# Performance work log

Hardware: AMD Instinct MI355X
Metric: run time of the kernel (lower is better)

The kernel has to match this reference:

```python
import jax, jax.numpy as jnp
import numpy as np

# CTBG circuit dims: units=[512,512,512], action_sz=6
UNIT1, UNIT2, UNIT3, ACTION = 512, 512, 512, 6
D_GPE_IN = UNIT1 * 3          # 1536  (striatum D1/D2/D3 blocks)
D_GPE_OUT = UNIT2 * 3         # 1536
D_GPI_IN = (UNIT1 + UNIT2) * 3  # 3072 (striatum + GPe/STN blocks)
D_GPI_OUT = UNIT2 * 3         # 1536
B = 16384


def setup_inputs() -> dict:
    key = jax.random.key(0)
    ks = jax.random.split(key, 12)
    x = jax.random.normal(ks[0], (B, D_GPE_IN), jnp.float32)
    # per-unit diagonal connectivity masks (unit_diags): [units, input_dim]
    gpe_mask = jax.random.bernoulli(ks[1], 0.5, (D_GPE_OUT, D_GPE_IN)).astype(jnp.float32)
    gpi_mask = jax.random.bernoulli(ks[2], 0.5, (D_GPI_OUT, D_GPI_IN)).astype(jnp.float32)
    # non-negative weights, uniform [0, 0.01) as in the TF initializer
    gpe_w = jax.random.uniform(ks[3], (D_GPE_IN, D_GPE_OUT), jnp.float32, 0.0, 0.01)
    gpe_b = jnp.zeros((D_GPE_OUT,), jnp.float32)
    gpi_w = jax.random.uniform(ks[4], (D_GPI_IN, D_GPI_OUT), jnp.float32, 0.0, 0.01)
    gpi_b = jnp.zeros((D_GPI_OUT,), jnp.float32)
    # Motor_cortex dense stack
    w1 = jax.random.normal(ks[5], (D_GPI_OUT, UNIT3), jnp.float32) / np.sqrt(D_GPI_OUT)
    b1 = jnp.zeros((UNIT3,), jnp.float32)
    w2 = jax.random.normal(ks[6], (UNIT3, UNIT3), jnp.float32) / np.sqrt(UNIT3)
    b2 = jnp.zeros((UNIT3,), jnp.float32)
    w3 = jax.random.normal(ks[7], (UNIT3, ACTION), jnp.float32) / np.sqrt(UNIT3)
    b3 = jnp.zeros((ACTION,), jnp.float32)
    return {"x": x, "gpe_mask": gpe_mask, "gpe_w": gpe_w, "gpe_b": gpe_b,
            "gpi_mask": gpi_mask, "gpi_w": gpi_w, "gpi_b": gpi_b,
            "w1": w1, "b1": b1, "w2": w2, "b2": b2, "w3": w3, "b3": b3}


def _masked_layer(x, mask, w, b):
    # TF original: p = transpose(matmul(diag(mask_u), x^T)) -> [B,U,I];
    #              f = diag_part(matmul(p, w)) + b
    # algebraically: f[b,u] = sum_i mask[u,i] * x[b,i] * w[i,u] + b[u]
    # which is a plain matmul against the element-wise masked weight.
    return x @ (w * mask.T) + b


def reference(x, gpe_mask, gpe_w, gpe_b, gpi_mask, gpi_w, gpi_b,
              w1, b1, w2, b2, w3, b3):
    gpe_out = _masked_layer(x, gpe_mask, gpe_w, gpe_b)          # [B, 1536]
    gpi_in = jnp.concatenate([x, gpe_out], axis=-1)              # [B, 3072]
    gpi_out = _masked_layer(gpi_in, gpi_mask, gpi_w, gpi_b)      # [B, 1536]
    h = jax.nn.relu(gpi_out @ w1 + b1)
    h = jax.nn.relu(h @ w2 + b2)
    return jax.nn.relu(h @ w3 + b3)                              # [B, 6]
```

## Files before the change

### kernel.cpp

```cpp
#include <hip/hip_runtime.h>
#include <stdint.h>


typedef __attribute__((ext_vector_type(8))) short short8;
typedef __attribute__((ext_vector_type(4))) float floatx4;

typedef const __attribute__((address_space(1))) void* gas1_cvp;
typedef __attribute__((address_space(3))) void* gas3_vp;

__device__ __forceinline__ void load_lds16(const void* g, void* s) {
    __builtin_amdgcn_global_load_lds((gas1_cvp)g, (gas3_vp)s, 16, 0, 0);
}

__device__ __forceinline__ unsigned short f2bf(float f) {
    unsigned int u = __float_as_uint(f);
    u = u + 0x7fffu + ((u >> 16) & 1u);
    return (unsigned short)(u >> 16);
}
__device__ __forceinline__ float bf2f(unsigned short h) {
    return __uint_as_float(((unsigned int)h) << 16);
}
__device__ __forceinline__ short8 cvt8(float4 a, float4 b) {
    short8 r;
    r[0] = (short)f2bf(a.x); r[1] = (short)f2bf(a.y);
    r[2] = (short)f2bf(a.z); r[3] = (short)f2bf(a.w);
    r[4] = (short)f2bf(b.x); r[5] = (short)f2bf(b.y);
    r[6] = (short)f2bf(b.z); r[7] = (short)f2bf(b.w);
    return r;
}

__device__ __forceinline__ void dev_prep_t(
        float (*tile)[65],
        const float* __restrict__ w, const float* __restrict__ mask,
        unsigned short* __restrict__ out,
        int ldw, int ldm, int ldo, int bx, int by) {
    int n0 = bx * 64;
    int k0 = by * 64;
    int t = threadIdx.x;
    int c4 = (t & 15) * 4;
    int r  = t >> 4;

    #pragma unroll
    for (int p = 0; p < 4; ++p) {
        int kk = r + p * 16;
        float4 v = *(const float4*)(w + (size_t)(k0 + kk) * ldw + n0 + c4);
        tile[c4 + 0][kk] = v.x;
        tile[c4 + 1][kk] = v.y;
        tile[c4 + 2][kk] = v.z;
        tile[c4 + 3][kk] = v.w;
    }
    __syncthreads();
    #pragma unroll
    for (int p = 0; p < 4; ++p) {
        int nn = r + p * 16;
        float mx = 1.f, my = 1.f, mz = 1.f, mw = 1.f;
        if (mask) {
            float4 m = *(const float4*)(mask + (size_t)(n0 + nn) * ldm + k0 + c4);
            mx = m.x; my = m.y; mz = m.z; mw = m.w;
        }
        ushort4 o;
        o.x = f2bf(tile[nn][c4 + 0] * mx);
        o.y = f2bf(tile[nn][c4 + 1] * my);
        o.z = f2bf(tile[nn][c4 + 2] * mz);
        o.w = f2bf(tile[nn][c4 + 3] * mw);
        *(ushort4*)(out + (size_t)(n0 + nn) * ldo + k0 + c4) = o;
    }
}

__device__ __forceinline__ void dev_prep_nt(
        float (*tile)[65],
        const float* __restrict__ w, const float* __restrict__ mask,
        unsigned short* __restrict__ out,
        int ldw, int ldm, int ldo, int bx, int by) {
    int j0 = bx * 64;
    int i0 = by * 64;
    int t = threadIdx.x;
    int c4 = (t & 15) * 4;
    int r  = t >> 4;

    #pragma unroll
    for (int p = 0; p < 4; ++p) {
        int jj = r + p * 16;
        float4 m = *(const float4*)(mask + (size_t)(j0 + jj) * ldm + i0 + c4);
        tile[c4 + 0][jj] = m.x;
        tile[c4 + 1][jj] = m.y;
        tile[c4 + 2][jj] = m.z;
        tile[c4 + 3][jj] = m.w;
    }
    __syncthreads();
    #pragma unroll
    for (int p = 0; p < 4; ++p) {
        int ii = r + p * 16;
        float4 v = *(const float4*)(w + (size_t)(i0 + ii) * ldw + j0 + c4);
        ushort4 o;
        o.x = f2bf(v.x * tile[ii][c4 + 0]);
        o.y = f2bf(v.y * tile[ii][c4 + 1]);
        o.z = f2bf(v.z * tile[ii][c4 + 2]);
        o.w = f2bf(v.w * tile[ii][c4 + 3]);
        *(ushort4*)(out + (size_t)(i0 + ii) * ldo + j0 + c4) = o;
    }
}

__global__ __launch_bounds__(256) void prep_all_kernel(
        const float* __restrict__ gpe_w, const float* __restrict__ gpe_mask,
        const float* __restrict__ gpi_w, const float* __restrict__ gpi_mask,
        const float* __restrict__ w1, const float* __restrict__ w2,
        unsigned short* __restrict__ wi_topnt, unsigned short* __restrict__ wibot_ui,
        unsigned short* __restrict__ we_nt, unsigned short* __restrict__ w1t,
        unsigned short* __restrict__ w2t) {
    __shared__ float tile[64][65];
    int b = blockIdx.x;
    if (b < 576) {
        dev_prep_nt(tile, gpi_w, gpi_mask, wi_topnt, 1536, 3072, 1536,
                    b % 24, b / 24);
    } else if (b < 1152) {
        int lb = b - 576;
        dev_prep_nt(tile, gpi_w + (size_t)1536 * 1536, gpi_mask + 1536, wibot_ui,
                    1536, 3072, 1536, lb % 24, lb / 24);
    } else if (b < 1728) {
        int lb = b - 1152;
        dev_prep_nt(tile, gpe_w, gpe_mask, we_nt, 1536, 1536, 1536,
                    lb % 24, lb / 24);
    } else if (b < 1920) {
        int lb = b - 1728;
        dev_prep_t(tile, w1, nullptr, w1t, 512, 0, 1536, lb % 8, lb / 8);
    } else {
        int lb = b - 1920;
        dev_prep_t(tile, w2, nullptr, w2t, 512, 0, 512, lb % 8, lb / 8);
    }
}

__device__ __forceinline__ void dev_combine_pipe(
        unsigned short* As, unsigned short* Bs,
        const unsigned short* __restrict__ A0,
        const unsigned short* __restrict__ B0,
        const unsigned short* __restrict__ A1,
        const unsigned short* __restrict__ B1,
        unsigned short* __restrict__ C,
        int nt0, int ntTot, int bx, int by) {
    const int m0 = by * 64;
    const int n0 = bx * 128;
    const int t    = threadIdx.x;
    const int lane = t & 63;
    const int w    = t >> 6;
    const int wm   = w >> 1;
    const int wn   = w & 1;
    const int lm   = lane & 15;
    const int lq   = lane >> 4;

    const int srow = lane >> 2;
    const int scol = (lane & 3) * 8;

    size_t ag_off[2];
    int rbA[2];
    #pragma unroll
    for (int i = 0; i < 2; ++i) {
        ag_off[i] = (size_t)(m0 + w * 16 + srow) * 1536 + i * 32 + scol;
        rbA[i]    = i * 2048 + w * 512;
    }
    size_t bg_off[4];
    int rbB[4];
    #pragma unroll
    for (int i = 0; i < 4; ++i) {
        int rows = w * 32 + (i >> 1) * 16;
        bg_off[i] = (size_t)(n0 + rows + srow) * 1536 + (i & 1) * 32 + scol;
        rbB[i]    = (i & 1) * 4096 + rows * 32;
    }

    int aro[2][2], bro[2][4];
    #pragma unroll
    for (int ks = 0; ks < 2; ++ks) {
        #pragma unroll
        for (int mi = 0; mi < 2; ++mi)
            aro[ks][mi] = ks * 2048 + (wm * 32 + mi * 16 + lm) * 32 + lq * 8;
        #pragma unroll
        for (int ni = 0; ni < 4; ++ni)
            bro[ks][ni] = ks * 4096 + (wn * 64 + ni * 16 + lm) * 32 + lq * 8;
    }

    floatx4 acc[2][4] = {};

    auto stage = [&](int s, int nb) {
        const unsigned short* Ab;
        const unsigned short* Bb;
        int kk;
        if (s < nt0) { Ab = A0; Bb = B0; kk = s << 6; }
        else         { Ab = A1; Bb = B1; kk = (s - nt0) << 6; }
        #pragma unroll
        for (int i = 0; i < 2; ++i)
            load_lds16(Ab + ag_off[i] + kk, As + nb * 4096 + rbA[i]);
        #pragma unroll
        for (int i = 0; i < 4; ++i)
            load_lds16(Bb + bg_off[i] + kk, Bs + nb * 8192 + rbB[i]);
    };

    stage(0, 0);
    __syncthreads();

    int buf = 0;
    for (int tt = 0; tt < ntTot; ++tt) {
        if (tt + 1 < ntTot) stage(tt + 1, buf ^ 1);
        const int cA = buf * 4096, cB = buf * 8192;
        #pragma unroll
        for (int ks = 0; ks < 2; ++ks) {
            short8 af[2], bf8[4];
            #pragma unroll
            for (int mi = 0; mi < 2; ++mi)
                af[mi] = *(const short8*)(As + cA + aro[ks][mi]);
            #pragma unroll
            for (int ni = 0; ni < 4; ++ni)
                bf8[ni] = *(const short8*)(Bs + cB + bro[ks][ni]);
            #pragma unroll
            for (int mi = 0; mi < 2; ++mi)
                #pragma unroll
                for (int ni = 0; ni < 4; ++ni)
                    acc[mi][ni] = __builtin_amdgcn_mfma_f32_16x16x32_bf16(
                        af[mi], bf8[ni], acc[mi][ni], 0, 0, 0);
        }
        if (tt + 1 < ntTot) __syncthreads();
        buf ^= 1;
    }

    #pragma unroll
    for (int mi = 0; mi < 2; ++mi) {
        int rbase = m0 + wm * 32 + mi * 16 + lq * 4;
        #pragma unroll
        for (int ni = 0; ni < 4; ++ni) {
            int cc = n0 + wn * 64 + ni * 16 + lm;
            #pragma unroll
            for (int r = 0; r < 4; ++r)
                C[(size_t)(rbase + r) * 1536 + cc] = f2bf(acc[mi][ni][r]);
        }
    }
}

__global__ __launch_bounds__(256) void combineA_kernel(
        const unsigned short* __restrict__ w1t,
        const unsigned short* __restrict__ wibot_ui,
        unsigned short* __restrict__ t1) {
    __shared__ unsigned short As[2 * 4096];
    __shared__ unsigned short Bs[2 * 8192];
    int b = blockIdx.x;
    dev_combine_pipe(As, Bs, w1t, wibot_ui, w1t, wibot_ui, t1,
                     24, 24, b % 12, b / 12);
}

__device__ __forceinline__ void dev_bvec2(
        const float* __restrict__ gpi_b, const float* __restrict__ gpe_b,
        const unsigned short* __restrict__ w1t,
        const unsigned short* __restrict__ t1,
        const float* __restrict__ b1, float* __restrict__ b1c, int blk) {
    int n = blk * 4 + (threadIdx.x >> 6);
    int lane = threadIdx.x & 63;
    const unsigned short* r1 = w1t + (size_t)n * 1536;
    const unsigned short* r2 = t1  + (size_t)n * 1536;
    float s = 0.f;
    for (int i = lane; i < 1536; i += 64)
        s += gpi_b[i] * bf2f(r1[i]) + gpe_b[i] * bf2f(r2[i]);
    #pragma unroll
    for (int off = 32; off; off >>= 1) s += __shfl_down(s, off, 64);
    if (lane == 0) b1c[n] = b1[n] + s;
}

__global__ __launch_bounds__(256) void combineB_kernel(
        const unsigned short* __restrict__ w1t,
        const unsigned short* __restrict__ wi_topnt,
        const unsigned short* __restrict__ t1,
        const unsigned short* __restrict__ we_nt,
        unsigned short* __restrict__ w1ct,
        const float* __restrict__ gpi_b, const float* __restrict__ gpe_b,
        const float* __restrict__ b1, float* __restrict__ b1c) {
    __shared__ unsigned short As[2 * 4096];
    __shared__ unsigned short Bs[2 * 8192];
    int b = blockIdx.x;
    if (b < 96) {
        dev_combine_pipe(As, Bs, w1t, wi_topnt, t1, we_nt, w1ct,
                         24, 48, b % 12, b / 12);
    } else {
        dev_bvec2(gpi_b, gpe_b, w1t, t1, b1, b1c, b - 96);
    }
}

__global__ __launch_bounds__(256) void gemm_a32_kernel(
        const float* __restrict__ A,
        const unsigned short* __restrict__ Bt,
        const float* __restrict__ bias,
        unsigned short* __restrict__ C,
        int K, int lda, int ldc) {
    __shared__ unsigned short As[2 * 8192];
    __shared__ unsigned short Bs[2 * 8192];

    const int bid = blockIdx.x;
    const int loc = bid >> 3;
    const int m0 = ((bid & 7) * 16 + (loc >> 2)) * 128;
    const int n0 = (loc & 3) * 128;

    const int t    = threadIdx.x;
    const int lane = t & 63;
    const int w    = t >> 6;
    const int wm   = w >> 1;
    const int wn   = w & 1;
    const int lm   = lane & 15;
    const int lq   = lane >> 4;

    const int srow = lane >> 2;
    const int scol = (lane & 3) * 8;

    const float* ag[4];
    const unsigned short* bg[4];
    int rb[4];
    int awr[4];
    #pragma unroll
    for (int i = 0; i < 4; ++i) {
        int rows = w * 32 + (i >> 1) * 16;
        ag[i]  = A  + (size_t)(m0 + rows + srow) * lda + (i & 1) * 32 + scol;
        bg[i]  = Bt + (size_t)(n0 + rows + srow) * K   + (i & 1) * 32 + scol;
        rb[i]  = (i & 1) * 4096 + rows * 32;
        awr[i] = (i & 1) * 4096 + (rows + srow) * 32 + scol;
    }

    int aro[2][4], bro[2][4];
    #pragma unroll
    for (int ks = 0; ks < 2; ++ks)
        #pragma unroll
        for (int i = 0; i < 4; ++i) {
            aro[ks][i] = ks * 4096 + (wm * 64 + i * 16 + lm) * 32 + lq * 8;
            bro[ks][i] = ks * 4096 + (wn * 64 + i * 16 + lm) * 32 + lq * 8;
        }

    floatx4 acc[4][4] = {};
    float4 ra[4][2];

    #pragma unroll
    for (int i = 0; i < 4; ++i) load_lds16(bg[i], Bs + rb[i]);
    #pragma unroll
    for (int i = 0; i < 4; ++i) {
        ra[i][0] = *(const float4*)(ag[i]);
        ra[i][1] = *(const float4*)(ag[i] + 4);
    }
    #pragma unroll
    for (int i = 0; i < 4; ++i)
        *(short8*)(As + awr[i]) = cvt8(ra[i][0], ra[i][1]);
    __syncthreads();

    const int nt = K >> 6;
    int buf = 0;
    for (int tt = 0; tt < nt; ++tt) {
        const int kn = (tt + 1) << 6;
        const int more = kn < K;
        if (more) {
            const int nb = (buf ^ 1) * 8192;
            #pragma unroll
            for (int i = 0; i < 4; ++i)
                load_lds16(bg[i] + kn, Bs + nb + rb[i]);
            #pragma unroll
            for (int i = 0; i < 4; ++i) {
                ra[i][0] = *(const float4*)(ag[i] + kn);
                ra[i][1] = *(const float4*)(ag[i] + kn + 4);
            }
        }
        const int cb = buf * 8192;
        #pragma unroll
        for (int ks = 0; ks < 2; ++ks) {
            short8 af[4], bf8[4];
            #pragma unroll
            for (int i = 0; i < 4; ++i) {
                af[i]  = *(const short8*)(As + cb + aro[ks][i]);
                bf8[i] = *(const short8*)(Bs + cb + bro[ks][i]);
            }
            #pragma unroll
            for (int mi = 0; mi < 4; ++mi)
                #pragma unroll
                for (int ni = 0; ni < 4; ++ni)
                    acc[mi][ni] = __builtin_amdgcn_mfma_f32_16x16x32_bf16(
                        af[mi], bf8[ni], acc[mi][ni], 0, 0, 0);
        }
        if (more) {
            const int nb = (buf ^ 1) * 8192;
            #pragma unroll
            for (int i = 0; i < 4; ++i)
                *(short8*)(As + nb + awr[i]) = cvt8(ra[i][0], ra[i][1]);
            __syncthreads();
        }
        buf ^= 1;
    }

    float bv[4];
    #pragma unroll
    for (int ni = 0; ni < 4; ++ni) bv[ni] = bias[n0 + wn * 64 + ni * 16 + lm];

    #pragma unroll
    for (int mi = 0; mi < 4; ++mi) {
        int rbase = m0 + wm * 64 + mi * 16 + lq * 4;
        #pragma unroll
        for (int ni = 0; ni < 4; ++ni) {
            int cc = n0 + wn * 64 + ni * 16 + lm;
            #pragma unroll
            for (int r = 0; r < 4; ++r) {
                float v = fmaxf(acc[mi][ni][r] + bv[ni], 0.f);
                C[(size_t)(rbase + r) * ldc + cc] = f2bf(v);
            }
        }
    }
}

__global__ __launch_bounds__(256) void gemm_bt_kernel(
        const unsigned short* __restrict__ A,
        const unsigned short* __restrict__ Bt,
        const float* __restrict__ bias,
        unsigned short* __restrict__ C,
        int K, int lda, int ldc) {
    __shared__ unsigned short As[2 * 8192];
    __shared__ unsigned short Bs[2 * 8192];

    const int bid = blockIdx.x;
    const int loc = bid >> 3;
    const int m0 = ((bid & 7) * 16 + (loc >> 2)) * 128;
    const int n0 = (loc & 3) * 128;

    const int t    = threadIdx.x;
    const int lane = t & 63;
    const int w    = t >> 6;
    const int wm   = w >> 1;
    const int wn   = w & 1;
    const int lm   = lane & 15;
    const int lq   = lane >> 4;

    const int srow = lane >> 2;
    const int scol = (lane & 3) * 8;

    const unsigned short* ag[4];
    const unsigned short* bg[4];
    int rb[4];
    #pragma unroll
    for (int i = 0; i < 4; ++i) {
        int rows = w * 32 + (i >> 1) * 16;
        ag[i] = A  + (size_t)(m0 + rows + srow) * lda + (i & 1) * 32 + scol;
        bg[i] = Bt + (size_t)(n0 + rows + srow) * K   + (i & 1) * 32 + scol;
        rb[i] = (i & 1) * 4096 + rows * 32;
    }

    int aro[2][4], bro[2][4];
    #pragma unroll
    for (int ks = 0; ks < 2; ++ks)
        #pragma unroll
        for (int i = 0; i < 4; ++i) {
            aro[ks][i] = ks * 4096 + (wm * 64 + i * 16 + lm) * 32 + lq * 8;
            bro[ks][i] = ks * 4096 + (wn * 64 + i * 16 + lm) * 32 + lq * 8;
        }

    floatx4 acc[4][4] = {};

    #pragma unroll
    for (int i = 0; i < 4; ++i) {
        load_lds16(ag[i], As + rb[i]);
        load_lds16(bg[i], Bs + rb[i]);
    }
    __syncthreads();

    const int nt = K >> 6;
    int buf = 0;
    for (int tt = 0; tt < nt; ++tt) {
        const int kn = (tt + 1) << 6;
        const int more = kn < K;
        if (more) {
            const int nb = (buf ^ 1) * 8192;
            #pragma unroll
            for (int i = 0; i < 4; ++i) {
                load_lds16(ag[i] + kn, As + nb + rb[i]);
                load_lds16(bg[i] + kn, Bs + nb + rb[i]);
            }
        }
        const int cb = buf * 8192;
        #pragma unroll
        for (int ks = 0; ks < 2; ++ks) {
            short8 af[4], bf8[4];
            #pragma unroll
            for (int i = 0; i < 4; ++i) {
                af[i]  = *(const short8*)(As + cb + aro[ks][i]);
                bf8[i] = *(const short8*)(Bs + cb + bro[ks][i]);
            }
            #pragma unroll
            for (int mi = 0; mi < 4; ++mi)
                #pragma unroll
                for (int ni = 0; ni < 4; ++ni)
                    acc[mi][ni] = __builtin_amdgcn_mfma_f32_16x16x32_bf16(
                        af[mi], bf8[ni], acc[mi][ni], 0, 0, 0);
        }
        if (more) __syncthreads();
        buf ^= 1;
    }

    float bv[4];
    #pragma unroll
    for (int ni = 0; ni < 4; ++ni) bv[ni] = bias[n0 + wn * 64 + ni * 16 + lm];

    #pragma unroll
    for (int mi = 0; mi < 4; ++mi) {
        int rbase = m0 + wm * 64 + mi * 16 + lq * 4;
        #pragma unroll
        for (int ni = 0; ni < 4; ++ni) {
            int cc = n0 + wn * 64 + ni * 16 + lm;
            #pragma unroll
            for (int r = 0; r < 4; ++r) {
                float v = fmaxf(acc[mi][ni][r] + bv[ni], 0.f);
                C[(size_t)(rbase + r) * ldc + cc] = f2bf(v);
            }
        }
    }
}

__global__ void head_kernel(const unsigned short* __restrict__ h,
                            const float* __restrict__ w3,
                            const float* __restrict__ b3,
                            float* __restrict__ out) {
    int row = blockIdx.x * 4 + (threadIdx.x >> 6);
    int lane = threadIdx.x & 63;
    const unsigned short* hp = h + (size_t)row * 512 + lane * 8;
    ushort4 ha = *(const ushort4*)(hp);
    ushort4 hb = *(const ushort4*)(hp + 4);
    float hv[8] = {bf2f(ha.x), bf2f(ha.y), bf2f(ha.z), bf2f(ha.w),
                   bf2f(hb.x), bf2f(hb.y), bf2f(hb.z), bf2f(hb.w)};
    const float* wp = w3 + lane * 48;
    float s[6] = {0.f, 0.f, 0.f, 0.f, 0.f, 0.f};
    #pragma unroll
    for (int j = 0; j < 8; ++j)
        #pragma unroll
        for (int a = 0; a < 6; ++a)
            s[a] += hv[j] * wp[j * 6 + a];
    #pragma unroll
    for (int a = 0; a < 6; ++a)
        #pragma unroll
        for (int off = 32; off; off >>= 1)
            s[a] += __shfl_down(s[a], off, 64);
    if (lane == 0) {
        #pragma unroll
        for (int a = 0; a < 6; ++a)
            out[(size_t)row * 6 + a] = fmaxf(s[a] + b3[a], 0.f);
    }
}

extern "C" void kernel_launch(void* const* d_in, const int* in_sizes, int n_in,
                              void* d_out, int out_size, void* d_ws, size_t ws_size,
                              hipStream_t stream) {
    const float* x        = (const float*)d_in[0];
    const float* gpe_mask = (const float*)d_in[1];
    const float* gpe_w    = (const float*)d_in[2];
    const float* gpe_b    = (const float*)d_in[3];
    const float* gpi_mask = (const float*)d_in[4];
    const float* gpi_w    = (const float*)d_in[5];
    const float* gpi_b    = (const float*)d_in[6];
    const float* w1       = (const float*)d_in[7];
    const float* b1       = (const float*)d_in[8];
    const float* w2       = (const float*)d_in[9];
    const float* b2       = (const float*)d_in[10];
    const float* w3       = (const float*)d_in[11];
    const float* b3       = (const float*)d_in[12];
    float* out = (float*)d_out;

    char* ws = (char*)d_ws;
    unsigned short* h1        = (unsigned short*)(ws);
    unsigned short* h2        = (unsigned short*)(ws + 16777216);
    unsigned short* wi_topnt  = (unsigned short*)(ws + 33554432);
    unsigned short* wibot_ui  = (unsigned short*)(ws + 38273024);
    unsigned short* we_nt     = (unsigned short*)(ws + 42991616);
    unsigned short* t1        = (unsigned short*)(ws + 47710208);
    unsigned short* w1t       = (unsigned short*)(ws + 49283072);
    unsigned short* w2t       = (unsigned short*)(ws + 50855936);
    unsigned short* w1ct      = (unsigned short*)(ws + 51380224);
    float*          b1c       = (float*)(ws + 52953088);

    prep_all_kernel<<<dim3(1984), dim3(256), 0, stream>>>(
        gpe_w, gpe_mask, gpi_w, gpi_mask, w1, w2,
        wi_topnt, wibot_ui, we_nt, w1t, w2t);

    combineA_kernel<<<dim3(96), dim3(256), 0, stream>>>(w1t, wibot_ui, t1);

    combineB_kernel<<<dim3(224), dim3(256), 0, stream>>>(
        w1t, wi_topnt, t1, we_nt, w1ct, gpi_b, gpe_b, b1, b1c);

    gemm_a32_kernel<<<dim3(512), dim3(256), 0, stream>>>(
        x, w1ct, b1c, h1, 1536, 1536, 512);
    gemm_bt_kernel<<<dim3(512), dim3(256), 0, stream>>>(
        h1, w2t, b2, h2, 512, 512, 512);
    head_kernel<<<dim3(16384 / 4), dim3(256), 0, stream>>>(h2, w3, b3, out);
}
```

Baseline: 346.3 us.

## Split-K the weight-combine GEMMs with fp32 atomic accumulation and finalize pass

The weight-folding GEMMs (combineA/combineB) launched only 96 blocks over a long K loop, leaving most CUs idle. They are now split along K into 512-wide chunks (288 and 576 blocks) that accumulate into fp32 buffers with atomic adds. The buffers are zeroed by extra blocks in the prep kernel, and a new finalize kernel converts the result to bf16 and computes the folded bias. The t1 intermediate stays in fp32 and is converted to bf16 when loaded into LDS. This costs an extra launch, atomic traffic and fp32 scratch memory, and makes the summation order nondeterministic.

```diff
diff --git a/kernel.cpp b/kernel.cpp
--- a/kernel.cpp
+++ b/kernel.cpp
@@ -107,7 +107,7 @@
         const float* __restrict__ w1, const float* __restrict__ w2,
         unsigned short* __restrict__ wi_topnt, unsigned short* __restrict__ wibot_ui,
         unsigned short* __restrict__ we_nt, unsigned short* __restrict__ w1t,
-        unsigned short* __restrict__ w2t) {
+        unsigned short* __restrict__ w2t, float* __restrict__ zero_base) {
     __shared__ float tile[64][65];
     int b = blockIdx.x;
     if (b < 576) {
@@ -124,20 +124,24 @@
     } else if (b < 1920) {
         int lb = b - 1728;
         dev_prep_t(tile, w1, nullptr, w1t, 512, 0, 1536, lb % 8, lb / 8);
-    } else {
+    } else if (b < 1984) {
         int lb = b - 1920;
         dev_prep_t(tile, w2, nullptr, w2t, 512, 0, 512, lb % 8, lb / 8);
-    }
-}
-
-__device__ __forceinline__ void dev_combine_pipe(
+    } else {
+        float4 z = {0.f, 0.f, 0.f, 0.f};
+        float* p = zero_base + (size_t)(b - 1984) * 4096 + threadIdx.x * 16;
+        #pragma unroll
+        for (int i = 0; i < 4; ++i) *(float4*)(p + i * 4) = z;
+    }
+}
+
+template <bool F32A>
+__device__ __forceinline__ void dev_combine_splitk(
         unsigned short* As, unsigned short* Bs,
-        const unsigned short* __restrict__ A0,
-        const unsigned short* __restrict__ B0,
-        const unsigned short* __restrict__ A1,
-        const unsigned short* __restrict__ B1,
-        unsigned short* __restrict__ C,
-        int nt0, int ntTot, int bx, int by) {
+        const void* __restrict__ Aop,
+        const unsigned short* __restrict__ B,
+        float* __restrict__ C,
+        int kbase, int ntl, int bx, int by) {
     const int m0 = by * 64;
     const int n0 = bx * 128;
     const int t    = threadIdx.x;
@@ -151,20 +155,21 @@
     const int srow = lane >> 2;
     const int scol = (lane & 3) * 8;
 
-    size_t ag_off[2];
-    int rbA[2];
+    size_t aidx[2];
+    int rbA[2], awr[2];
     #pragma unroll
     for (int i = 0; i < 2; ++i) {
-        ag_off[i] = (size_t)(m0 + w * 16 + srow) * 1536 + i * 32 + scol;
-        rbA[i]    = i * 2048 + w * 512;
-    }
-    size_t bg_off[4];
+        aidx[i] = (size_t)(m0 + w * 16 + srow) * 1536 + i * 32 + scol + kbase;
+        rbA[i]  = i * 2048 + w * 512;
+        awr[i]  = i * 2048 + (w * 16 + srow) * 32 + scol;
+    }
+    size_t bidx[4];
     int rbB[4];
     #pragma unroll
     for (int i = 0; i < 4; ++i) {
         int rows = w * 32 + (i >> 1) * 16;
-        bg_off[i] = (size_t)(n0 + rows + srow) * 1536 + (i & 1) * 32 + scol;
-        rbB[i]    = (i & 1) * 4096 + rows * 32;
+        bidx[i] = (size_t)(n0 + rows + srow) * 1536 + (i & 1) * 32 + scol + kbase;
+        rbB[i]  = (i & 1) * 4096 + rows * 32;
     }
 
     int aro[2][2], bro[2][4];
@@ -178,28 +183,51 @@
             bro[ks][ni] = ks * 4096 + (wn * 64 + ni * 16 + lm) * 32 + lq * 8;
     }
 
+    const float* Af = (const float*)Aop;
+    const unsigned short* Ab = (const unsigned short*)Aop;
+
     floatx4 acc[2][4] = {};
-
-    auto stage = [&](int s, int nb) {
-        const unsigned short* Ab;
-        const unsigned short* Bb;
-        int kk;
-        if (s < nt0) { Ab = A0; Bb = B0; kk = s << 6; }
-        else         { Ab = A1; Bb = B1; kk = (s - nt0) << 6; }
+    float4 ra[2][2];
+
+    #pragma unroll
+    for (int i = 0; i < 4; ++i) load_lds16(B + bidx[i], Bs + rbB[i]);
+    if (F32A) {
+        #pragma unroll
+        for (int i = 0; i < 2; ++i) {
+            ra[i][0] = *(const float4*)(Af + aidx[i]);
+            ra[i][1] = *(const float4*)(Af + aidx[i] + 4);
+        }
         #pragma unroll
         for (int i = 0; i < 2; ++i)
-            load_lds16(Ab + ag_off[i] + kk, As + nb * 4096 + rbA[i]);
-        #pragma unroll
-        for (int i = 0; i < 4; ++i)
-            load_lds16(Bb + bg_off[i] + kk, Bs + nb * 8192 + rbB[i]);
-    };
-
-    stage(0, 0);
+            *(short8*)(As + awr[i]) = cvt8(ra[i][0], ra[i][1]);
+    } else {
+        #pragma unroll
+        for (int i = 0; i < 2; ++i) load_lds16(Ab + aidx[i], As + rbA[i]);
+    }
     __syncthreads();
 
     int buf = 0;
-    for (int tt = 0; tt < ntTot; ++tt) {
-        if (tt + 1 < ntTot) stage(tt + 1, buf ^ 1);
+    for (int tt = 0; tt < ntl; ++tt) {
+        const int kn = (tt + 1) << 6;
+        const int more = tt + 1 < ntl;
+        if (more) {
+            const int nbA = (buf ^ 1) * 4096;
+            const int nbB = (buf ^ 1) * 8192;
+            #pragma unroll
+            for (int i = 0; i < 4; ++i)
+                load_lds16(B + bidx[i] + kn, Bs + nbB + rbB[i]);
+            if (F32A) {
+                #pragma unroll
+                for (int i = 0; i < 2; ++i) {
+                    ra[i][0] = *(const float4*)(Af + aidx[i] + kn);
+                    ra[i][1] = *(const float4*)(Af + aidx[i] + kn + 4);
+                }
+            } else {
+                #pragma unroll
+                for (int i = 0; i < 2; ++i)
+                    load_lds16(Ab + aidx[i] + kn, As + nbA + rbA[i]);
+            }
+        }
         const int cA = buf * 4096, cB = buf * 8192;
         #pragma unroll
         for (int ks = 0; ks < 2; ++ks) {
@@ -217,7 +245,15 @@
                     acc[mi][ni] = __builtin_amdgcn_mfma_f32_16x16x32_bf16(
                         af[mi], bf8[ni], acc[mi][ni], 0, 0, 0);
         }
-        if (tt + 1 < ntTot) __syncthreads();
+        if (more) {
+            if (F32A) {
+                const int nbA = (buf ^ 1) * 4096;
+                #pragma unroll
+                for (int i = 0; i < 2; ++i)
+                    *(short8*)(As + nbA + awr[i]) = cvt8(ra[i][0], ra[i][1]);
+            }
+            __syncthreads();
+        }
         buf ^= 1;
     }
 
@@ -229,7 +265,8 @@
             int cc = n0 + wn * 64 + ni * 16 + lm;
             #pragma unroll
             for (int r = 0; r < 4; ++r)
-                C[(size_t)(rbase + r) * 1536 + cc] = f2bf(acc[mi][ni][r]);
+                unsafeAtomicAdd(&C[(size_t)(rbase + r) * 1536 + cc],
+                                acc[mi][ni][r]);
         }
     }
 }
@@ -237,47 +274,63 @@
 __global__ __launch_bounds__(256) void combineA_kernel(
         const unsigned short* __restrict__ w1t,
         const unsigned short* __restrict__ wibot_ui,
-        unsigned short* __restrict__ t1) {
+        float* __restrict__ t1f) {
     __shared__ unsigned short As[2 * 4096];
     __shared__ unsigned short Bs[2 * 8192];
     int b = blockIdx.x;
-    dev_combine_pipe(As, Bs, w1t, wibot_ui, w1t, wibot_ui, t1,
-                     24, 24, b % 12, b / 12);
-}
-
-__device__ __forceinline__ void dev_bvec2(
-        const float* __restrict__ gpi_b, const float* __restrict__ gpe_b,
-        const unsigned short* __restrict__ w1t,
-        const unsigned short* __restrict__ t1,
-        const float* __restrict__ b1, float* __restrict__ b1c, int blk) {
-    int n = blk * 4 + (threadIdx.x >> 6);
-    int lane = threadIdx.x & 63;
-    const unsigned short* r1 = w1t + (size_t)n * 1536;
-    const unsigned short* r2 = t1  + (size_t)n * 1536;
-    float s = 0.f;
-    for (int i = lane; i < 1536; i += 64)
-        s += gpi_b[i] * bf2f(r1[i]) + gpe_b[i] * bf2f(r2[i]);
-    #pragma unroll
-    for (int off = 32; off; off >>= 1) s += __shfl_down(s, off, 64);
-    if (lane == 0) b1c[n] = b1[n] + s;
+    int s = b / 96;
+    int r = b % 96;
+    dev_combine_splitk<false>(As, Bs, w1t, wibot_ui, t1f,
+                              s * 512, 8, r % 12, r / 12);
 }
 
 __global__ __launch_bounds__(256) void combineB_kernel(
         const unsigned short* __restrict__ w1t,
         const unsigned short* __restrict__ wi_topnt,
-        const unsigned short* __restrict__ t1,
+        const float* __restrict__ t1f,
         const unsigned short* __restrict__ we_nt,
-        unsigned short* __restrict__ w1ct,
-        const float* __restrict__ gpi_b, const float* __restrict__ gpe_b,
-        const float* __restrict__ b1, float* __restrict__ b1c) {
+        float* __restrict__ w1cf) {
     __shared__ unsigned short As[2 * 4096];
     __shared__ unsigned short Bs[2 * 8192];
     int b = blockIdx.x;
-    if (b < 96) {
-        dev_combine_pipe(As, Bs, w1t, wi_topnt, t1, we_nt, w1ct,
-                         24, 48, b % 12, b / 12);
+    int c = b / 96;
+    int r = b % 96;
+    int kbase = (c % 3) * 512;
+    if (c < 3) {
+        dev_combine_splitk<false>(As, Bs, w1t, wi_topnt, w1cf,
+                                  kbase, 8, r % 12, r / 12);
     } else {
-        dev_bvec2(gpi_b, gpe_b, w1t, t1, b1, b1c, b - 96);
+        dev_combine_splitk<true>(As, Bs, t1f, we_nt, w1cf,
+                                 kbase, 8, r % 12, r / 12);
+    }
+}
+
+__global__ __launch_bounds__(256) void finalize_kernel(
+        const float* __restrict__ w1cf, unsigned short* __restrict__ w1ct,
+        const unsigned short* __restrict__ w1t, const float* __restrict__ t1f,
+        const float* __restrict__ gpi_b, const float* __restrict__ gpe_b,
+        const float* __restrict__ b1, float* __restrict__ b1c) {
+    int b = blockIdx.x;
+    if (b < 384) {
+        size_t base = (size_t)b * 2048 + threadIdx.x * 8;
+        float4 v0 = *(const float4*)(w1cf + base);
+        float4 v1 = *(const float4*)(w1cf + base + 4);
+        ushort4 o0, o1;
+        o0.x = f2bf(v0.x); o0.y = f2bf(v0.y); o0.z = f2bf(v0.z); o0.w = f2bf(v0.w);
+        o1.x = f2bf(v1.x); o1.y = f2bf(v1.y); o1.z = f2bf(v1.z); o1.w = f2bf(v1.w);
+        *(ushort4*)(w1ct + base) = o0;
+        *(ushort4*)(w1ct + base + 4) = o1;
+    } else {
+        int n = (b - 384) * 4 + (threadIdx.x >> 6);
+        int lane = threadIdx.x & 63;
+        const unsigned short* r1 = w1t + (size_t)n * 1536;
+        const float* r2 = t1f + (size_t)n * 1536;
+        float s = 0.f;
+        for (int i = lane; i < 1536; i += 64)
+            s += gpi_b[i] * bf2f(r1[i]) + gpe_b[i] * r2[i];
+        #pragma unroll
+        for (int off = 32; off; off >>= 1) s += __shfl_down(s, off, 64);
+        if (lane == 0) b1c[n] = b1[n] + s;
     }
 }
 
@@ -561,23 +614,27 @@
     char* ws = (char*)d_ws;
     unsigned short* h1        = (unsigned short*)(ws);
     unsigned short* h2        = (unsigned short*)(ws + 16777216);
+    float*          t1f       = (float*)(ws + 16777216);
+    float*          w1cf      = (float*)(ws + 19922944);
     unsigned short* wi_topnt  = (unsigned short*)(ws + 33554432);
     unsigned short* wibot_ui  = (unsigned short*)(ws + 38273024);
     unsigned short* we_nt     = (unsigned short*)(ws + 42991616);
-    unsigned short* t1        = (unsigned short*)(ws + 47710208);
-    unsigned short* w1t       = (unsigned short*)(ws + 49283072);
-    unsigned short* w2t       = (unsigned short*)(ws + 50855936);
-    unsigned short* w1ct      = (unsigned short*)(ws + 51380224);
-    float*          b1c       = (float*)(ws + 52953088);
-
-    prep_all_kernel<<<dim3(1984), dim3(256), 0, stream>>>(
+    unsigned short* w1t       = (unsigned short*)(ws + 47710208);
+    unsigned short* w2t       = (unsigned short*)(ws + 49283072);
+    unsigned short* w1ct      = (unsigned short*)(ws + 49807360);
+    float*          b1c       = (float*)(ws + 51380224);
+
+    prep_all_kernel<<<dim3(2368), dim3(256), 0, stream>>>(
         gpe_w, gpe_mask, gpi_w, gpi_mask, w1, w2,
-        wi_topnt, wibot_ui, we_nt, w1t, w2t);
-
-    combineA_kernel<<<dim3(96), dim3(256), 0, stream>>>(w1t, wibot_ui, t1);
-
-    combineB_kernel<<<dim3(224), dim3(256), 0, stream>>>(
-        w1t, wi_topnt, t1, we_nt, w1ct, gpi_b, gpe_b, b1, b1c);
+        wi_topnt, wibot_ui, we_nt, w1t, w2t, t1f);
+
+    combineA_kernel<<<dim3(288), dim3(256), 0, stream>>>(w1t, wibot_ui, t1f);
+
+    combineB_kernel<<<dim3(576), dim3(256), 0, stream>>>(
+        w1t, wi_topnt, t1f, we_nt, w1cf);
+
+    finalize_kernel<<<dim3(512), dim3(256), 0, stream>>>(
+        w1cf, w1ct, w1t, t1f, gpi_b, gpe_b, b1, b1c);
 
     gemm_a32_kernel<<<dim3(512), dim3(256), 0, stream>>>(
         x, w1ct, b1c, h1, 1536, 1536, 512);
```

Measured after the change: 322.4 us. -6.9%, faster.
